# Optimization experiments

Measured on AMD Instinct MI355X. Metric: run time of the kernel, lower is better.

## Reference

```python
import jax, jax.numpy as jnp
import numpy as np

NHEADS = 4   # attention heads (search_cfg.nheads)
WS = 7       # spatial search window side -> WS*WS candidates per query
PS = 3       # patch size for distance computation (search_cfg.ps)
K = 16       # top-k neighbors kept (search_cfg.k)


def layer_norm_2d(vid, w, b, eps=1e-6):
    # LayerNorm over channel dim at every (t,h,w) location; vid (B,T,C,H,W)
    mu = vid.mean(axis=2, keepdims=True)
    var = vid.var(axis=2, keepdims=True)
    y = (vid - mu) / jnp.sqrt(var + eps)
    return y * w[None, None, :, None, None] + b[None, None, :, None, None]


def conv1x1(vid, w, b):
    # 1x1 ConvQKV projection: vid (B,T,C,H,W), w (O,C)
    return jnp.einsum('btchw,oc->btohw', vid, w) + b[None, None, :, None, None]


def box_sum(x, ps):
    # sum over centered ps x ps patch (zero pad); x (..., H, W)
    r = ps // 2
    H, W = x.shape[-2], x.shape[-1]
    xp = jnp.pad(x, [(0, 0)] * (x.ndim - 2) + [(r, r), (r, r)])
    out = jnp.zeros_like(x)
    ah, aw = x.ndim - 2, x.ndim - 1
    for dy in range(ps):
        for dx in range(ps):
            s = jax.lax.dynamic_slice_in_dim(xp, dy, H, ah)
            s = jax.lax.dynamic_slice_in_dim(s, dx, W, aw)
            out = out + s
    return out


def nl_search(q, k):
    # patch-based non-local search: q,k (B,T,HD,c,H,W)
    B, T, HD, c, H, W = q.shape
    r = WS // 2
    kp = jnp.pad(k, ((0, 0),) * 4 + ((r, r), (r, r)))  # zero pad = invalid candidates score ~0
    offs = jnp.stack(jnp.meshgrid(jnp.arange(WS), jnp.arange(WS), indexing='ij'), -1).reshape(-1, 2)

    @jax.checkpoint
    def step(carry, off):
        dy, dx = off[0], off[1]
        ksh = jax.lax.dynamic_slice(kp, (0, 0, 0, 0, dy, dx), (B, T, HD, c, H, W))
        s = (q * ksh).sum(axis=3)      # pixel inner products (B,T,HD,H,W)
        s = box_sum(s, PS)             # patch inner products
        return carry, s

    _, scores = jax.lax.scan(step, 0, offs)        # (WS*WS,B,T,HD,H,W)
    scores = jnp.moveaxis(scores, 0, -1)           # (B,T,HD,H,W,WS*WS)
    dists, inds = jax.lax.top_k(scores, K)         # top-k neighbors per query
    return dists, inds


def nl_stack(v, weights, inds):
    # gather the K selected neighbor values, weighted; v (B,T,HD,c,H,W)
    B, T, HD, c, H, W = v.shape
    r = WS // 2
    vp = jnp.pad(v, ((0, 0),) * 4 + ((r, r), (r, r)))
    Hp, Wp = H + 2 * r, W + 2 * r
    row = jnp.arange(H)[:, None, None] + inds // WS   # (B,T,HD,H,W,K)
    col = jnp.arange(W)[None, :, None] + inds % WS
    lin = (row * Wp + col).reshape(B, T, HD, 1, H * W * K)
    vf = vp.reshape(B, T, HD, c, Hp * Wp)
    g = jnp.take_along_axis(vf, jnp.broadcast_to(lin, (B, T, HD, c, H * W * K)), axis=-1)
    g = g.reshape(B, T, HD, c, H, W, K)
    g = g * weights[:, :, :, None]                    # weight each neighbor
    # -> (B*T, HD*c, K, H, W) stack for Conv3d projection
    return jnp.transpose(g, (0, 1, 2, 3, 6, 4, 5)).reshape(B * T, HD * c, K, H, W)


def proj3d(stack, w, b):
    # Conv3d(io_dim, io_dim, (K,3,3), stride=(K,1,1), pad=(0,1,1), groups=NHEADS)
    out = jax.lax.conv_general_dilated(
        stack, w, window_strides=(K, 1, 1),
        padding=((0, 0), (1, 1), (1, 1)),
        dimension_numbers=('NCDHW', 'OIDHW', 'NCDHW'),
        feature_group_count=NHEADS)
    return out[:, :, 0] + b[None, :, None, None]


def setup_inputs() -> dict:
    key = jax.random.key(0)
    ks = jax.random.split(key, 8)
    B, T, C, H, W = 1, 4, 128, 96, 96
    sc = 1.0 / np.sqrt(C)
    inp = {
        'vid': jax.random.normal(ks[0], (B, T, C, H, W), jnp.float32),
        'ln_w': jnp.ones((C,), jnp.float32),
        'ln_b': jnp.zeros((C,), jnp.float32),
        'wq': jax.random.normal(ks[1], (C, C), jnp.float32) * sc,
        'bq': jnp.zeros((C,), jnp.float32),
        'wk': jax.random.normal(ks[2], (C, C), jnp.float32) * sc,
        'bk': jnp.zeros((C,), jnp.float32),
        'wv': jax.random.normal(ks[3], (C, C), jnp.float32) * sc,
        'bv': jnp.zeros((C,), jnp.float32),
        'proj_w': jax.random.normal(ks[4], (C, C // NHEADS, K, 3, 3), jnp.float32) * 0.02,
        'proj_b': jnp.zeros((C,), jnp.float32),
    }
    return inp


def reference(vid, ln_w, ln_b, wq, bq, wk, bk, wv, bv, proj_w, proj_b):
    B, T, C, H, W = vid.shape
    x = layer_norm_2d(vid, ln_w, ln_b)
    q = conv1x1(x, wq, bq)
    k = conv1x1(x, wk, bk)
    v = conv1x1(x, wv, bv)
    hd = lambda t: t.reshape(B, T, NHEADS, C // NHEADS, H, W)
    q, k, v = hd(q), hd(k), hd(v)
    dists, inds = nl_search(q, k)                 # k-NN search
    weights = jax.nn.softmax(dists, axis=-1)      # normalize over K
    stack = nl_stack(v, weights, inds)            # neighbor stacking
    out = proj3d(stack, proj_w, proj_b)           # conv projection collapses K
    return out.reshape(B, T, C, H, W)
```

## Files before the change

### kernel.cpp

```cpp
#include <hip/hip_runtime.h>


typedef float  f32x4  __attribute__((ext_vector_type(4)));
typedef __bf16 bf16x8 __attribute__((ext_vector_type(8)));

__device__ __forceinline__ float dpp_shr1(float x) {
  return __int_as_float(__builtin_amdgcn_update_dpp(0, __float_as_int(x), 0x111, 0xf, 0xf, false));
}
__device__ __forceinline__ float dpp_shl1(float x) {
  return __int_as_float(__builtin_amdgcn_update_dpp(0, __float_as_int(x), 0x101, 0xf, 0xf, false));
}

__global__ __launch_bounds__(256) void prep_kernel(
    const float* __restrict__ wq, const float* __restrict__ wk, const float* __restrict__ wv,
    const float* __restrict__ pw, float* __restrict__ Wt, __bf16* __restrict__ pwt,
    __bf16* __restrict__ wvh) {
  int idx = blockIdx.x * 256 + threadIdx.x;
  const int NPW = 4 * 16 * 9 * 32 * 32;
  if (idx < NPW) {
    int i  = idx & 31;
    int ol = (idx >> 5) & 31;
    int d  = (idx >> 10) % 9;
    int r  = (idx >> 10) / 9;
    int kd = r & 15;
    int g  = r >> 4;
    int o  = g * 32 + ol;
    pwt[idx] = (__bf16)pw[((o * 32 + i) * 16 + kd) * 9 + d];
  } else if (idx < NPW + 128 * 384) {
    int widx = idx - NPW;
    int o = widx % 384;
    int c = widx / 384;
    const float* __restrict__ src = (o < 128) ? wq : (o < 256 ? wk : wv);
    Wt[widx] = src[(o & 127) * 128 + c];
  } else {
    int vidx = idx - NPW - 128 * 384;
    if (vidx < 128 * 128) wvh[vidx] = (__bf16)wv[vidx];
  }
}

__global__ __launch_bounds__(64) void ln_stats_kernel(
    const float* __restrict__ vid, float* __restrict__ mu, float* __restrict__ rs) {
  int pix = blockIdx.x * 64 + threadIdx.x;
  int f = blockIdx.y;
  const float* __restrict__ vp = vid + (size_t)f * 128 * 9216 + pix;
  float s = 0.f, s2 = 0.f;
  #pragma unroll 8
  for (int c = 0; c < 128; ++c) { float x = vp[(size_t)c * 9216]; s += x; s2 += x * x; }
  float m_ = s * (1.f / 128.f);
  float v_ = fmaxf(s2 * (1.f / 128.f) - m_ * m_, 0.f);
  mu[f * 9216 + pix] = m_;
  rs[f * 9216 + pix] = rsqrtf(v_ + 1e-6f);
}

__global__ __launch_bounds__(256) void xbf_kernel(
    const float* __restrict__ vid, const float* __restrict__ mu, const float* __restrict__ rs,
    const float* __restrict__ lnw, const float* __restrict__ lnb, __bf16* __restrict__ xbf) {
  __shared__ __align__(16) __bf16 tile[128 * 128];
  __shared__ float muL[128], rsL[128], lwS[128], lbS[128];
  int t = threadIdx.x;
  int pf = blockIdx.x * 128;
  int f = blockIdx.y;
  if (t < 128) { muL[t] = mu[f * 9216 + pf + t]; rsL[t] = rs[f * 9216 + pf + t]; }
  else { lwS[t - 128] = lnw[t - 128]; lbS[t - 128] = lnb[t - 128]; }
  __syncthreads();
  #pragma unroll 4
  for (int it = 0; it < 16; ++it) {
    int idx = it * 256 + t;
    int c = idx >> 5, p4 = idx & 31;
    float4 v = *(const float4*)&vid[((size_t)(f * 128 + c)) * 9216 + pf + p4 * 4];
    float xs[4] = {v.x, v.y, v.z, v.w};
    #pragma unroll
    for (int i = 0; i < 4; ++i) {
      int pix = p4 * 4 + i;
      float xn = (xs[i] - muL[pix]) * rsL[pix] * lwS[c] + lbS[c];
      int cp = c ^ (((pix >> 2) & 7) << 3);
      tile[pix * 128 + cp] = (__bf16)xn;
    }
  }
  __syncthreads();
  int pix = t >> 1, half = t & 1;
  __bf16* __restrict__ dst = xbf + ((size_t)(f * 9216) + pf + pix) * 128 + half * 64;
  #pragma unroll
  for (int cc = 0; cc < 8; ++cc) {
    int chunk = half * 8 + cc;
    int cs = chunk ^ ((pix >> 2) & 7);
    *(int4*)&dst[cc * 8] = *(const int4*)&tile[pix * 128 + cs * 8];
  }
}

__global__ __launch_bounds__(256) void qk_gemm_kernel(
    const float* __restrict__ vid, const float* __restrict__ mu, const float* __restrict__ rs,
    const float* __restrict__ lnw, const float* __restrict__ lnb,
    const float* __restrict__ Wt, const float* __restrict__ bq, const float* __restrict__ bk,
    float* __restrict__ qb, float* __restrict__ kb) {
  __shared__ __align__(16) float Xs[32][128];
  __shared__ __align__(16) float Ws[32][128];
  __shared__ float muL[128], rsL[128], lwS[128], lbS[128];
  int tid = threadIdx.x;
  int mt = blockIdx.y;
  int N0 = blockIdx.x * 128;
  int f  = mt / 72;
  int pf = (mt % 72) * 128;

  if (tid < 128) {
    muL[tid] = mu[f * 9216 + pf + tid];
    rsL[tid] = rs[f * 9216 + pf + tid];
  } else {
    int t2 = tid - 128;
    lwS[t2] = lnw[t2];
    lbS[t2] = lnb[t2];
  }

  int tx = tid & 15, ty = tid >> 4;
  int m0 = ty * 8;
  int sm = tid & 127;
  int sk0 = tid >> 7;
  float acc[8][8];
  #pragma unroll
  for (int a = 0; a < 8; ++a)
    #pragma unroll
    for (int b = 0; b < 8; ++b) acc[a][b] = 0.f;

  const size_t vbase = (size_t)f * 128 * 9216 + pf;
  float xr[16], wr[16];

  #pragma unroll
  for (int it = 0; it < 16; ++it) {
    int kk = sk0 + 2 * it;
    xr[it] = vid[vbase + (size_t)kk * 9216 + sm];
    wr[it] = Wt[(size_t)kk * 384 + N0 + sm];
  }
  __syncthreads();
  #pragma unroll
  for (int it = 0; it < 16; ++it) {
    int kk = sk0 + 2 * it;
    Xs[kk][sm] = (xr[it] - muL[sm]) * rsL[sm] * lwS[kk] + lbS[kk];
    Ws[kk][sm] = wr[it];
  }
  __syncthreads();

  for (int kc = 0; kc < 4; ++kc) {
    if (kc < 3) {
      #pragma unroll
      for (int it = 0; it < 16; ++it) {
        int kk = sk0 + 2 * it;
        int c = (kc + 1) * 32 + kk;
        xr[it] = vid[vbase + (size_t)c * 9216 + sm];
        wr[it] = Wt[(size_t)c * 384 + N0 + sm];
      }
    }
    #pragma unroll 2
    for (int kk = 0; kk < 32; ++kk) {
      float xa[8], wa[8];
      *(float4*)&xa[0] = *(const float4*)&Xs[kk][m0];
      *(float4*)&xa[4] = *(const float4*)&Xs[kk][m0 + 4];
      *(float4*)&wa[0] = *(const float4*)&Ws[kk][tx * 4];
      *(float4*)&wa[4] = *(const float4*)&Ws[kk][64 + tx * 4];
      #pragma unroll
      for (int a = 0; a < 8; ++a)
        #pragma unroll
        for (int b = 0; b < 8; ++b)
          acc[a][b] = fmaf(xa[a], wa[b], acc[a][b]);
    }
    if (kc < 3) {
      __syncthreads();
      #pragma unroll
      for (int it = 0; it < 16; ++it) {
        int kk = sk0 + 2 * it;
        int c = (kc + 1) * 32 + kk;
        Xs[kk][sm] = (xr[it] - muL[sm]) * rsL[sm] * lwS[c] + lbS[c];
        Ws[kk][sm] = wr[it];
      }
      __syncthreads();
    }
  }

  int sel = blockIdx.x;
  int nlo = tx * 4, nhi = 64 + tx * 4;
  int hlo = nlo >> 5, clo = nlo & 31;
  int hhi = nhi >> 5, chi = nhi & 31;
  const float* __restrict__ bias = (sel == 0) ? bq : bk;
  float* __restrict__ dst = (sel == 0) ? qb : kb;
  float4 blo = make_float4(bias[nlo], bias[nlo + 1], bias[nlo + 2], bias[nlo + 3]);
  float4 bhi = make_float4(bias[nhi], bias[nhi + 1], bias[nhi + 2], bias[nhi + 3]);
  size_t base_lo = (size_t)(f * 4 + hlo) * 9216 * 32 + clo;
  size_t base_hi = (size_t)(f * 4 + hhi) * 9216 * 32 + chi;
  #pragma unroll
  for (int a = 0; a < 8; ++a) {
    size_t poff = (size_t)(pf + m0 + a) * 32;
    *(float4*)&dst[base_lo + poff] = make_float4(acc[a][0] + blo.x, acc[a][1] + blo.y,
                                                 acc[a][2] + blo.z, acc[a][3] + blo.w);
    *(float4*)&dst[base_hi + poff] = make_float4(acc[a][4] + bhi.x, acc[a][5] + bhi.y,
                                                 acc[a][6] + bhi.z, acc[a][7] + bhi.w);
  }
}

__global__ __launch_bounds__(256) void vmfma_kernel(
    const __bf16* __restrict__ xbf, const __bf16* __restrict__ wvh,
    const float* __restrict__ bv, __bf16* __restrict__ vbbf) {
  __shared__ __align__(16) __bf16 XL[64 * 128];
  __shared__ __align__(16) __bf16 WL[128 * 128];
  int t = threadIdx.x;
  int bid = blockIdx.x;
  int f = bid / 144;
  int pf = (bid % 144) * 64;

  #pragma unroll
  for (int i = 0; i < 4; ++i) {
    int idx = i * 256 + t;
    int pix = idx >> 4, ck = idx & 15;
    int4 val = *(const int4*)&xbf[((size_t)(f * 9216) + pf + pix) * 128 + ck * 8];
    *(int4*)&XL[pix * 128 + ((ck ^ (pix & 7)) << 3)] = val;
  }
  #pragma unroll
  for (int i = 0; i < 8; ++i) {
    int idx = i * 256 + t;
    int o = idx >> 4, ck = idx & 15;
    int4 val = *(const int4*)&wvh[o * 128 + ck * 8];
    *(int4*)&WL[o * 128 + ((ck ^ (o & 7)) << 3)] = val;
  }
  __syncthreads();

  int lane = t & 63, w = t >> 6;
  int wm = w >> 1, wn = w & 1;
  int kg = lane >> 4, lr = lane & 15;
  f32x4 acc[2][4];
  #pragma unroll
  for (int mf = 0; mf < 2; ++mf)
    #pragma unroll
    for (int nf = 0; nf < 4; ++nf) acc[mf][nf] = (f32x4)(0.0f);

  #pragma unroll
  for (int kc = 0; kc < 4; ++kc) {
    int ck = kc * 4 + kg;
    bf16x8 a[2], b[4];
    #pragma unroll
    for (int mf = 0; mf < 2; ++mf) {
      int pix = wm * 32 + mf * 16 + lr;
      a[mf] = *(const bf16x8*)&XL[pix * 128 + ((ck ^ (pix & 7)) << 3)];
    }
    #pragma unroll
    for (int nf = 0; nf < 4; ++nf) {
      int o = wn * 64 + nf * 16 + lr;
      b[nf] = *(const bf16x8*)&WL[o * 128 + ((ck ^ (o & 7)) << 3)];
    }
    #pragma unroll
    for (int mf = 0; mf < 2; ++mf)
      #pragma unroll
      for (int nf = 0; nf < 4; ++nf)
        acc[mf][nf] = __builtin_amdgcn_mfma_f32_16x16x32_bf16(a[mf], b[nf], acc[mf][nf], 0, 0, 0);
  }

  #pragma unroll
  for (int mf = 0; mf < 2; ++mf) {
    #pragma unroll
    for (int nf = 0; nf < 4; ++nf) {
      int o = wn * 64 + nf * 16 + lr;
      int head = o >> 5, c = o & 31;
      float bias = bv[o];
      #pragma unroll
      for (int j = 0; j < 4; ++j) {
        int pix = wm * 32 + mf * 16 + kg * 4 + j;
        vbbf[((size_t)((f * 4 + head) * 9216) + pf + pix) * 32 + c] =
            (__bf16)(acc[mf][nf][j] + bias);
      }
    }
  }
}

__global__ __launch_bounds__(256, 3) void search_kernel(
    const float* __restrict__ qb, const float* __restrict__ kb,
    float* __restrict__ wgtb, int* __restrict__ indb) {
  __shared__ __align__(16) float klds[16 * 22 * 32];
  __shared__ float slds[7][256];
  int tid = threadIdx.x;
  int th = blockIdx.y;
  int tile = blockIdx.x;
  int iy0 = (tile / 7) * 14, ix0 = (tile % 7) * 14;
  const float* __restrict__ kbase = kb + (size_t)th * 9216 * 32;

  #pragma unroll
  for (int it = 0; it < 11; ++it) {
    int i = it * 256 + tid;
    int r = i / 176, rem = i % 176;
    int col = rem >> 3, c4 = rem & 7;
    int gy = iy0 - 4 + r, gx = ix0 - 4 + col;
    float4 val = make_float4(0.f, 0.f, 0.f, 0.f);
    if ((unsigned)gy < 96u && (unsigned)gx < 96u)
      val = *(const float4*)&kbase[(size_t)(gy * 96 + gx) * 32 + c4 * 4];
    int p = r * 22 + col;
    *(float4*)&klds[p * 32 + ((c4 ^ (p & 7)) << 2)] = val;
  }

  int sy = tid >> 4, sx = tid & 15;
  int qy = iy0 - 1 + sy, qx = ix0 - 1 + sx;
  bool qok = (unsigned)qy < 96u && (unsigned)qx < 96u;
  float4 qv[8];
  #pragma unroll
  for (int j = 0; j < 8; ++j) qv[j] = make_float4(0.f, 0.f, 0.f, 0.f);
  if (qok) {
    const float* __restrict__ qp = qb + ((size_t)th * 9216 + qy * 96 + qx) * 32;
    #pragma unroll
    for (int j = 0; j < 8; ++j) qv[j] = *(const float4*)&qp[j * 4];
  }
  bool inner = (sy >= 1) && (sy <= 14) && (sx >= 1) && (sx <= 14) && qok;

  float tv[16]; int tix[16];
  #pragma unroll
  for (int j = 0; j < 16; ++j) { tv[j] = -3.0e38f; tix[j] = 0; }
  __syncthreads();

  #pragma unroll 1
  for (int dy = 0; dy < 7; ++dy) {
    if (dy > 0) {
      if (tid < 176) {
        int col = tid >> 3, c4 = tid & 7;
        int r = dy + 15;
        int gy = iy0 - 4 + r, gx = ix0 - 4 + col;
        float4 val = make_float4(0.f, 0.f, 0.f, 0.f);
        if ((unsigned)gy < 96u && (unsigned)gx < 96u)
          val = *(const float4*)&kbase[(size_t)(gy * 96 + gx) * 32 + c4 * 4];
        int p = (r & 15) * 22 + col;
        *(float4*)&klds[p * 32 + ((c4 ^ (p & 7)) << 2)] = val;
      }
      __syncthreads();
    }
    float h[7];
    #pragma unroll
    for (int dx = 0; dx < 7; ++dx) {
      int p = ((sy + dy) & 15) * 22 + (sx + dx);
      const float* __restrict__ kp = &klds[p * 32];
      int sw = p & 7;
      float sdot = 0.f;
      #pragma unroll
      for (int j = 0; j < 8; ++j) {
        float4 kq = *(const float4*)&kp[(j ^ sw) << 2];
        sdot += qv[j].x * kq.x + qv[j].y * kq.y + qv[j].z * kq.z + qv[j].w * kq.w;
      }
      h[dx] = sdot + dpp_shr1(sdot) + dpp_shl1(sdot);
      slds[dx][tid] = h[dx];
    }
    __syncthreads();
    if (inner) {
      #pragma unroll
      for (int dx = 0; dx < 7; ++dx) {
        float sc = h[dx] + slds[dx][tid - 16] + slds[dx][tid + 16];
        int oi = dy * 7 + dx;
        float cv = sc; int ci = oi;
        #pragma unroll
        for (int j = 0; j < 16; ++j) {
          bool gt = cv > tv[j];
          float mx = fmaxf(tv[j], cv);
          float mn = fminf(tv[j], cv);
          int nt = gt ? ci : tix[j];
          ci = gt ? tix[j] : ci;
          tv[j] = mx; cv = mn; tix[j] = nt;
        }
      }
    }
  }

  if (inner) {
    float mx = tv[0];
    float e[16], ssum = 0.f;
    #pragma unroll
    for (int j = 0; j < 16; ++j) { e[j] = __expf(tv[j] - mx); ssum += e[j]; }
    float inv = 1.f / ssum;
    size_t base = ((size_t)th * 9216 + qy * 96 + qx) * 16;
    #pragma unroll
    for (int j = 0; j < 4; ++j) {
      *(float4*)&wgtb[base + j * 4] =
          make_float4(e[j*4] * inv, e[j*4+1] * inv, e[j*4+2] * inv, e[j*4+3] * inv);
      *(int4*)&indb[base + j * 4] = make_int4(tix[j*4], tix[j*4+1], tix[j*4+2], tix[j*4+3]);
    }
  }
}

#define STAGE_A(BUF, VR, WC) do {                                              \
  if (gact) {                                                                  \
    __bf16 tmp_[32];                                                           \
    _Pragma("unroll")                                                          \
    for (int wv_ = 0; wv_ < 4; ++wv_) {                                        \
      unsigned uu_[4] = {(unsigned)VR[wv_].x, (unsigned)VR[wv_].y,             \
                         (unsigned)VR[wv_].z, (unsigned)VR[wv_].w};            \
      _Pragma("unroll")                                                        \
      for (int j2_ = 0; j2_ < 4; ++j2_) {                                      \
        float lo_ = __uint_as_float(uu_[j2_] << 16);                           \
        float hi_ = __uint_as_float(uu_[j2_] & 0xffff0000u);                   \
        tmp_[wv_ * 8 + j2_ * 2]     = (__bf16)(lo_ * (WC));                    \
        tmp_[wv_ * 8 + j2_ * 2 + 1] = (__bf16)(hi_ * (WC));                    \
      }                                                                        \
    }                                                                          \
    __bf16* dst_ = &(BUF)[tid * 32];                                           \
    int sela_ = (tid >> 1) & 3;                                                \
    *(int4*)&dst_[(0 ^ sela_) << 3] = *(const int4*)&tmp_[0];                  \
    *(int4*)&dst_[(1 ^ sela_) << 3] = *(const int4*)&tmp_[8];                  \
    *(int4*)&dst_[(2 ^ sela_) << 3] = *(const int4*)&tmp_[16];                 \
    *(int4*)&dst_[(3 ^ sela_) << 3] = *(const int4*)&tmp_[24];                 \
  }                                                                            \
} while (0)

#define STAGE_B(BUF, KD) do {                                                  \
  const __bf16* __restrict__ bsrc_ = pwt + (size_t)(g * 16 + (KD)) * 9216;     \
  _Pragma("unroll")                                                            \
  for (int itb_ = 0; itb_ < 3; ++itb_) {                                       \
    int i_ = itb_ * 512 + tid;                                                 \
    if (i_ < 1152) {                                                           \
      int row_ = i_ >> 2, c_ = i_ & 3;                                         \
      *(int4*)&(BUF)[row_ * 32 + ((c_ ^ ((row_ >> 1) & 3)) << 3)] =            \
          *(const int4*)&bsrc_[row_ * 32 + c_ * 8];                            \
    }                                                                          \
  }                                                                            \
} while (0)

#define GATHER(VR, WC, IND, W) do {                                            \
  int ind_ = (IND);                                                            \
  VR[0] = VR[1] = VR[2] = VR[3] = make_int4(0, 0, 0, 0);                       \
  if (inb) {                                                                   \
    int ny_ = gy + ind_ / 7 - 3, nx_ = gx + ind_ % 7 - 3;                      \
    if ((unsigned)ny_ < 96u && (unsigned)nx_ < 96u) {                          \
      const int4* __restrict__ vp_ =                                           \
          (const int4*)(vbase + (size_t)(ny_ * 96 + nx_) * 32);                \
      VR[0] = vp_[0]; VR[1] = vp_[1]; VR[2] = vp_[2]; VR[3] = vp_[3];          \
    }                                                                          \
  }                                                                            \
  WC = (W);                                                                    \
} while (0)

#define MFMA_PHASE(AB, BB) do {                                                \
  _Pragma("unroll")                                                            \
  for (int dx2_ = 0; dx2_ < 3; ++dx2_) {                                       \
    bf16x8 a_[4];                                                              \
    _Pragma("unroll")                                                          \
    for (int r_ = 0; r_ < 4; ++r_) {                                           \
      int p_ = (wid * 2 + r_) * 18 + lr + dx2_;                                \
      a_[r_] = *(const bf16x8*)&(AB)[p_ * 32 + ((kg ^ ((p_ >> 1) & 3)) << 3)]; \
    }                                                                          \
    _Pragma("unroll")                                                          \
    for (int dy2_ = 0; dy2_ < 3; ++dy2_) {                                     \
      int d_ = dy2_ * 3 + dx2_;                                                \
      bf16x8 b0_ = *(const bf16x8*)&(BB)[(d_ * 32 + lr) * 32 + bswz];          \
      bf16x8 b1_ = *(const bf16x8*)&(BB)[(d_ * 32 + 16 + lr) * 32 + bswz];     \
      acc[0][0] = __builtin_amdgcn_mfma_f32_16x16x32_bf16(a_[dy2_],     b0_, acc[0][0], 0, 0, 0); \
      acc[0][1] = __builtin_amdgcn_mfma_f32_16x16x32_bf16(a_[dy2_],     b1_, acc[0][1], 0, 0, 0); \
      acc[1][0] = __builtin_amdgcn_mfma_f32_16x16x32_bf16(a_[dy2_ + 1], b0_, acc[1][0], 0, 0, 0); \
      acc[1][1] = __builtin_amdgcn_mfma_f32_16x16x32_bf16(a_[dy2_ + 1], b1_, acc[1][1], 0, 0, 0); \
    }                                                                          \
  }                                                                            \
} while (0)

__global__ __launch_bounds__(512) void proj_kernel(
    const __bf16* __restrict__ vb, const float* __restrict__ wgtb, const int* __restrict__ indb,
    const __bf16* __restrict__ pwt, const float* __restrict__ pb, float* __restrict__ outp) {
  __shared__ __align__(16) __bf16 Albuf[2][324 * 32];
  __shared__ __align__(16) __bf16 Blbuf[2][288 * 32];
  int tid = threadIdx.x;
  int bid = blockIdx.x;
  int wg = (bid & 7) * 72 + (bid >> 3);
  int th = wg / 36;
  int tile = wg % 36;
  int g = th & 3;
  int ty0 = (tile / 6) * 16, tx0 = (tile % 6) * 16;
  int lane = tid & 63, wid = tid >> 6;
  int kg = lane >> 4, lr = lane & 15;
  int bswz = (kg ^ ((lr >> 1) & 3)) << 3;

  bool gact = tid < 324;
  int ry = tid / 18, rx = tid % 18;
  int gy = ty0 - 1 + ry, gx = tx0 - 1 + rx;
  bool inb = gact && (unsigned)gy < 96u && (unsigned)gx < 96u;
  const __bf16* __restrict__ vbase = vb + (size_t)th * 9216 * 32;
  size_t pxoff = inb ? (size_t)(gy * 96 + gx) : 0;
  const int*   __restrict__ ibase = indb + ((size_t)th * 9216 + pxoff) * 16;
  const float* __restrict__ wbase = wgtb + ((size_t)th * 9216 + pxoff) * 16;

  f32x4 acc[2][2];
  acc[0][0] = (f32x4)(0.0f); acc[0][1] = (f32x4)(0.0f);
  acc[1][0] = (f32x4)(0.0f); acc[1][1] = (f32x4)(0.0f);

  int4 iw_i = make_int4(0, 0, 0, 0);
  float4 iw_w = make_float4(0.f, 0.f, 0.f, 0.f);
  int4 vr0[4], vr1[4];
  float wc0 = 0.f, wc1 = 0.f;

  if (inb) {
    iw_i = *(const int4*)&ibase[0];
    iw_w = *(const float4*)&wbase[0];
  }
  GATHER(vr0, wc0, iw_i.x, iw_w.x);
  STAGE_A(Albuf[0], vr0, wc0);
  STAGE_B(Blbuf[0], 0);
  GATHER(vr1, wc1, iw_i.y, iw_w.y);
  __syncthreads();

  #pragma unroll 1
  for (int kq = 0; kq < 4; ++kq) {
    int k4 = kq * 4;
    STAGE_A(Albuf[1], vr1, wc1);
    STAGE_B(Blbuf[1], k4 + 1);
    GATHER(vr0, wc0, iw_i.z, iw_w.z);
    MFMA_PHASE(Albuf[0], Blbuf[0]);
    __syncthreads();
    STAGE_A(Albuf[0], vr0, wc0);
    STAGE_B(Blbuf[0], k4 + 2);
    GATHER(vr1, wc1, iw_i.w, iw_w.w);
    MFMA_PHASE(Albuf[1], Blbuf[1]);
    __syncthreads();
    STAGE_A(Albuf[1], vr1, wc1);
    STAGE_B(Blbuf[1], k4 + 3);
    if (kq < 3) {
      if (inb) {
        iw_i = *(const int4*)&ibase[k4 + 4];
        iw_w = *(const float4*)&wbase[k4 + 4];
      }
      GATHER(vr0, wc0, iw_i.x, iw_w.x);
    }
    MFMA_PHASE(Albuf[0], Blbuf[0]);
    __syncthreads();
    if (kq < 3) {
      STAGE_A(Albuf[0], vr0, wc0);
      STAGE_B(Blbuf[0], k4 + 4);
      GATHER(vr1, wc1, iw_i.y, iw_w.y);
    }
    MFMA_PHASE(Albuf[1], Blbuf[1]);
    __syncthreads();
  }

  int x0 = tx0 + kg * 4;
  int f = th >> 2;
  #pragma unroll
  for (int mt = 0; mt < 2; ++mt) {
    int y = ty0 + wid * 2 + mt;
    #pragma unroll
    for (int nt = 0; nt < 2; ++nt) {
      int o = g * 32 + nt * 16 + lr;
      float bias = pb[o];
      float4 res = make_float4(acc[mt][nt][0] + bias, acc[mt][nt][1] + bias,
                               acc[mt][nt][2] + bias, acc[mt][nt][3] + bias);
      *(float4*)&outp[(size_t)(f * 128 + o) * 9216 + y * 96 + x0] = res;
    }
  }
}

extern "C" void kernel_launch(void* const* d_in, const int* in_sizes, int n_in,
                              void* d_out, int out_size, void* d_ws, size_t ws_size,
                              hipStream_t stream) {
  const float* vid = (const float*)d_in[0];
  const float* lnw = (const float*)d_in[1];
  const float* lnb = (const float*)d_in[2];
  const float* wq  = (const float*)d_in[3];
  const float* bq  = (const float*)d_in[4];
  const float* wk  = (const float*)d_in[5];
  const float* bk  = (const float*)d_in[6];
  const float* wv_ = (const float*)d_in[7];
  const float* bv  = (const float*)d_in[8];
  const float* pw  = (const float*)d_in[9];
  const float* pb  = (const float*)d_in[10];
  float* outp = (float*)d_out;

  const size_t SZ_T  = (size_t)16 * 9216 * 32 * 4;
  const size_t SZ_TB = (size_t)16 * 9216 * 32 * 2;
  const size_t SZ_W  = (size_t)16 * 9216 * 16 * 4;
  const size_t SZ_WT = 128 * 384 * 4;
  const size_t SZ_PW = (size_t)4 * 16 * 9 * 32 * 32 * 2;
  const size_t SZ_MU = (size_t)4 * 9216 * 4;
  const size_t SZ_XB = (size_t)4 * 9216 * 128 * 2;
  const size_t SZ_WV = 128 * 128 * 2;

  char* p = (char*)d_ws;
  float* qb = (float*)p;        p += SZ_T;
  float* kb = (float*)p;        p += SZ_T;
  __bf16* vbbf = (__bf16*)p;    p += SZ_TB;
  float* wgtb = (float*)p;      p += SZ_W;
  int*   indb = (int*)p;        p += SZ_W;
  float* Wt = (float*)p;        p += SZ_WT;
  __bf16* pwt = (__bf16*)p;     p += SZ_PW;
  float* mu = (float*)p;        p += SZ_MU;
  float* rs = (float*)p;        p += SZ_MU;
  __bf16* xbf = (__bf16*)p;     p += SZ_XB;
  __bf16* wvh = (__bf16*)p;

  prep_kernel<<<2560, 256, 0, stream>>>(wq, wk, wv_, pw, Wt, pwt, wvh);
  ln_stats_kernel<<<dim3(144, 4), 64, 0, stream>>>(vid, mu, rs);
  xbf_kernel<<<dim3(72, 4), 256, 0, stream>>>(vid, mu, rs, lnw, lnb, xbf);
  qk_gemm_kernel<<<dim3(2, 288), 256, 0, stream>>>(vid, mu, rs, lnw, lnb, Wt, bq, bk, qb, kb);
  vmfma_kernel<<<576, 256, 0, stream>>>(xbf, wvh, bv, vbbf);
  search_kernel<<<dim3(49, 16), 256, 0, stream>>>(qb, kb, wgtb, indb);
  proj_kernel<<<576, 512, 0, stream>>>(vbbf, wgtb, indb, pwt, pb, outp);
}
```

Measured before the change: 212.8 us.

## Merge independent kernels into two block-dispatched fat kernels

```diff
diff --git a/kernel.cpp b/kernel.cpp
--- a/kernel.cpp
+++ b/kernel.cpp
@@ -52,326 +52,333 @@
   rs[f * 9216 + pix] = rsqrtf(v_ + 1e-6f);
 }
 
-__global__ __launch_bounds__(256) void xbf_kernel(
-    const float* __restrict__ vid, const float* __restrict__ mu, const float* __restrict__ rs,
-    const float* __restrict__ lnw, const float* __restrict__ lnb, __bf16* __restrict__ xbf) {
-  __shared__ __align__(16) __bf16 tile[128 * 128];
-  __shared__ float muL[128], rsL[128], lwS[128], lbS[128];
-  int t = threadIdx.x;
-  int pf = blockIdx.x * 128;
-  int f = blockIdx.y;
-  if (t < 128) { muL[t] = mu[f * 9216 + pf + t]; rsL[t] = rs[f * 9216 + pf + t]; }
-  else { lwS[t - 128] = lnw[t - 128]; lbS[t - 128] = lnb[t - 128]; }
-  __syncthreads();
-  #pragma unroll 4
-  for (int it = 0; it < 16; ++it) {
-    int idx = it * 256 + t;
-    int c = idx >> 5, p4 = idx & 31;
-    float4 v = *(const float4*)&vid[((size_t)(f * 128 + c)) * 9216 + pf + p4 * 4];
-    float xs[4] = {v.x, v.y, v.z, v.w};
-    #pragma unroll
-    for (int i = 0; i < 4; ++i) {
-      int pix = p4 * 4 + i;
-      float xn = (xs[i] - muL[pix]) * rsL[pix] * lwS[c] + lbS[c];
-      int cp = c ^ (((pix >> 2) & 7) << 3);
-      tile[pix * 128 + cp] = (__bf16)xn;
-    }
-  }
-  __syncthreads();
-  int pix = t >> 1, half = t & 1;
-  __bf16* __restrict__ dst = xbf + ((size_t)(f * 9216) + pf + pix) * 128 + half * 64;
-  #pragma unroll
-  for (int cc = 0; cc < 8; ++cc) {
-    int chunk = half * 8 + cc;
-    int cs = chunk ^ ((pix >> 2) & 7);
-    *(int4*)&dst[cc * 8] = *(const int4*)&tile[pix * 128 + cs * 8];
-  }
-}
-
-__global__ __launch_bounds__(256) void qk_gemm_kernel(
+__global__ __launch_bounds__(256) void fat1_kernel(
     const float* __restrict__ vid, const float* __restrict__ mu, const float* __restrict__ rs,
     const float* __restrict__ lnw, const float* __restrict__ lnb,
     const float* __restrict__ Wt, const float* __restrict__ bq, const float* __restrict__ bk,
-    float* __restrict__ qb, float* __restrict__ kb) {
-  __shared__ __align__(16) float Xs[32][128];
-  __shared__ __align__(16) float Ws[32][128];
-  __shared__ float muL[128], rsL[128], lwS[128], lbS[128];
+    float* __restrict__ qb, float* __restrict__ kb, __bf16* __restrict__ xbf) {
+  __shared__ __align__(16) char smem[34816];
   int tid = threadIdx.x;
-  int mt = blockIdx.y;
-  int N0 = blockIdx.x * 128;
-  int f  = mt / 72;
-  int pf = (mt % 72) * 128;
-
-  if (tid < 128) {
-    muL[tid] = mu[f * 9216 + pf + tid];
-    rsL[tid] = rs[f * 9216 + pf + tid];
+  int bid = blockIdx.x;
+  if (bid < 576) {
+    float* Xs  = (float*)smem;
+    float* Ws  = (float*)(smem + 16384);
+    float* muL = (float*)(smem + 32768);
+    float* rsL = muL + 128;
+    float* lwS = muL + 256;
+    float* lbS = muL + 384;
+    int sel = bid & 1;
+    int mt  = bid >> 1;
+    int N0 = sel * 128;
+    int f  = mt / 72;
+    int pf = (mt % 72) * 128;
+
+    if (tid < 128) {
+      muL[tid] = mu[f * 9216 + pf + tid];
+      rsL[tid] = rs[f * 9216 + pf + tid];
+    } else {
+      int t2 = tid - 128;
+      lwS[t2] = lnw[t2];
+      lbS[t2] = lnb[t2];
+    }
+
+    int tx = tid & 15, ty = tid >> 4;
+    int m0 = ty * 8;
+    int sm = tid & 127;
+    int sk0 = tid >> 7;
+    float acc[8][8];
+    #pragma unroll
+    for (int a = 0; a < 8; ++a)
+      #pragma unroll
+      for (int b = 0; b < 8; ++b) acc[a][b] = 0.f;
+
+    const size_t vbase = (size_t)f * 128 * 9216 + pf;
+    float xr[16], wr[16];
+
+    #pragma unroll
+    for (int it = 0; it < 16; ++it) {
+      int kk = sk0 + 2 * it;
+      xr[it] = vid[vbase + (size_t)kk * 9216 + sm];
+      wr[it] = Wt[(size_t)kk * 384 + N0 + sm];
+    }
+    __syncthreads();
+    #pragma unroll
+    for (int it = 0; it < 16; ++it) {
+      int kk = sk0 + 2 * it;
+      Xs[kk * 128 + sm] = (xr[it] - muL[sm]) * rsL[sm] * lwS[kk] + lbS[kk];
+      Ws[kk * 128 + sm] = wr[it];
+    }
+    __syncthreads();
+
+    for (int kc = 0; kc < 4; ++kc) {
+      if (kc < 3) {
+        #pragma unroll
+        for (int it = 0; it < 16; ++it) {
+          int kk = sk0 + 2 * it;
+          int c = (kc + 1) * 32 + kk;
+          xr[it] = vid[vbase + (size_t)c * 9216 + sm];
+          wr[it] = Wt[(size_t)c * 384 + N0 + sm];
+        }
+      }
+      #pragma unroll 2
+      for (int kk = 0; kk < 32; ++kk) {
+        float xa[8], wa[8];
+        *(float4*)&xa[0] = *(const float4*)&Xs[kk * 128 + m0];
+        *(float4*)&xa[4] = *(const float4*)&Xs[kk * 128 + m0 + 4];
+        *(float4*)&wa[0] = *(const float4*)&Ws[kk * 128 + tx * 4];
+        *(float4*)&wa[4] = *(const float4*)&Ws[kk * 128 + 64 + tx * 4];
+        #pragma unroll
+        for (int a = 0; a < 8; ++a)
+          #pragma unroll
+          for (int b = 0; b < 8; ++b)
+            acc[a][b] = fmaf(xa[a], wa[b], acc[a][b]);
+      }
+      if (kc < 3) {
+        __syncthreads();
+        #pragma unroll
+        for (int it = 0; it < 16; ++it) {
+          int kk = sk0 + 2 * it;
+          int c = (kc + 1) * 32 + kk;
+          Xs[kk * 128 + sm] = (xr[it] - muL[sm]) * rsL[sm] * lwS[c] + lbS[c];
+          Ws[kk * 128 + sm] = wr[it];
+        }
+        __syncthreads();
+      }
+    }
+
+    int nlo = tx * 4, nhi = 64 + tx * 4;
+    int hlo = nlo >> 5, clo = nlo & 31;
+    int hhi = nhi >> 5, chi = nhi & 31;
+    const float* __restrict__ bias = (sel == 0) ? bq : bk;
+    float* __restrict__ dst = (sel == 0) ? qb : kb;
+    float4 blo = make_float4(bias[nlo], bias[nlo + 1], bias[nlo + 2], bias[nlo + 3]);
+    float4 bhi = make_float4(bias[nhi], bias[nhi + 1], bias[nhi + 2], bias[nhi + 3]);
+    size_t base_lo = (size_t)(f * 4 + hlo) * 9216 * 32 + clo;
+    size_t base_hi = (size_t)(f * 4 + hhi) * 9216 * 32 + chi;
+    #pragma unroll
+    for (int a = 0; a < 8; ++a) {
+      size_t poff = (size_t)(pf + m0 + a) * 32;
+      *(float4*)&dst[base_lo + poff] = make_float4(acc[a][0] + blo.x, acc[a][1] + blo.y,
+                                                   acc[a][2] + blo.z, acc[a][3] + blo.w);
+      *(float4*)&dst[base_hi + poff] = make_float4(acc[a][4] + bhi.x, acc[a][5] + bhi.y,
+                                                   acc[a][6] + bhi.z, acc[a][7] + bhi.w);
+    }
   } else {
-    int t2 = tid - 128;
-    lwS[t2] = lnw[t2];
-    lbS[t2] = lnb[t2];
+    __bf16* tile = (__bf16*)smem;
+    float* muL = (float*)(smem + 32768);
+    float* rsL = muL + 128;
+    float* lwS = muL + 256;
+    float* lbS = muL + 384;
+    int r = bid - 576;
+    int pf = (r % 72) * 128;
+    int f = r / 72;
+    if (tid < 128) { muL[tid] = mu[f * 9216 + pf + tid]; rsL[tid] = rs[f * 9216 + pf + tid]; }
+    else { lwS[tid - 128] = lnw[tid - 128]; lbS[tid - 128] = lnb[tid - 128]; }
+    __syncthreads();
+    #pragma unroll 4
+    for (int it = 0; it < 16; ++it) {
+      int idx = it * 256 + tid;
+      int c = idx >> 5, p4 = idx & 31;
+      float4 v = *(const float4*)&vid[((size_t)(f * 128 + c)) * 9216 + pf + p4 * 4];
+      float xs[4] = {v.x, v.y, v.z, v.w};
+      #pragma unroll
+      for (int i = 0; i < 4; ++i) {
+        int pix = p4 * 4 + i;
+        float xn = (xs[i] - muL[pix]) * rsL[pix] * lwS[c] + lbS[c];
+        int cp = c ^ (((pix >> 2) & 7) << 3);
+        tile[pix * 128 + cp] = (__bf16)xn;
+      }
+    }
+    __syncthreads();
+    int pix = tid >> 1, half = tid & 1;
+    __bf16* __restrict__ dst = xbf + ((size_t)(f * 9216) + pf + pix) * 128 + half * 64;
+    #pragma unroll
+    for (int cc = 0; cc < 8; ++cc) {
+      int chunk = half * 8 + cc;
+      int cs = chunk ^ ((pix >> 2) & 7);
+      *(int4*)&dst[cc * 8] = *(const int4*)&tile[pix * 128 + cs * 8];
+    }
   }
-
-  int tx = tid & 15, ty = tid >> 4;
-  int m0 = ty * 8;
-  int sm = tid & 127;
-  int sk0 = tid >> 7;
-  float acc[8][8];
-  #pragma unroll
-  for (int a = 0; a < 8; ++a)
-    #pragma unroll
-    for (int b = 0; b < 8; ++b) acc[a][b] = 0.f;
-
-  const size_t vbase = (size_t)f * 128 * 9216 + pf;
-  float xr[16], wr[16];
-
-  #pragma unroll
-  for (int it = 0; it < 16; ++it) {
-    int kk = sk0 + 2 * it;
-    xr[it] = vid[vbase + (size_t)kk * 9216 + sm];
-    wr[it] = Wt[(size_t)kk * 384 + N0 + sm];
-  }
-  __syncthreads();
-  #pragma unroll
-  for (int it = 0; it < 16; ++it) {
-    int kk = sk0 + 2 * it;
-    Xs[kk][sm] = (xr[it] - muL[sm]) * rsL[sm] * lwS[kk] + lbS[kk];
-    Ws[kk][sm] = wr[it];
-  }
-  __syncthreads();
-
-  for (int kc = 0; kc < 4; ++kc) {
-    if (kc < 3) {
-      #pragma unroll
-      for (int it = 0; it < 16; ++it) {
-        int kk = sk0 + 2 * it;
-        int c = (kc + 1) * 32 + kk;
-        xr[it] = vid[vbase + (size_t)c * 9216 + sm];
-        wr[it] = Wt[(size_t)c * 384 + N0 + sm];
-      }
-    }
-    #pragma unroll 2
-    for (int kk = 0; kk < 32; ++kk) {
-      float xa[8], wa[8];
-      *(float4*)&xa[0] = *(const float4*)&Xs[kk][m0];
-      *(float4*)&xa[4] = *(const float4*)&Xs[kk][m0 + 4];
-      *(float4*)&wa[0] = *(const float4*)&Ws[kk][tx * 4];
-      *(float4*)&wa[4] = *(const float4*)&Ws[kk][64 + tx * 4];
-      #pragma unroll
-      for (int a = 0; a < 8; ++a)
-        #pragma unroll
-        for (int b = 0; b < 8; ++b)
-          acc[a][b] = fmaf(xa[a], wa[b], acc[a][b]);
-    }
-    if (kc < 3) {
-      __syncthreads();
-      #pragma unroll
-      for (int it = 0; it < 16; ++it) {
-        int kk = sk0 + 2 * it;
-        int c = (kc + 1) * 32 + kk;
-        Xs[kk][sm] = (xr[it] - muL[sm]) * rsL[sm] * lwS[c] + lbS[c];
-        Ws[kk][sm] = wr[it];
-      }
-      __syncthreads();
-    }
-  }
-
-  int sel = blockIdx.x;
-  int nlo = tx * 4, nhi = 64 + tx * 4;
-  int hlo = nlo >> 5, clo = nlo & 31;
-  int hhi = nhi >> 5, chi = nhi & 31;
-  const float* __restrict__ bias = (sel == 0) ? bq : bk;
-  float* __restrict__ dst = (sel == 0) ? qb : kb;
-  float4 blo = make_float4(bias[nlo], bias[nlo + 1], bias[nlo + 2], bias[nlo + 3]);
-  float4 bhi = make_float4(bias[nhi], bias[nhi + 1], bias[nhi + 2], bias[nhi + 3]);
-  size_t base_lo = (size_t)(f * 4 + hlo) * 9216 * 32 + clo;
-  size_t base_hi = (size_t)(f * 4 + hhi) * 9216 * 32 + chi;
-  #pragma unroll
-  for (int a = 0; a < 8; ++a) {
-    size_t poff = (size_t)(pf + m0 + a) * 32;
-    *(float4*)&dst[base_lo + poff] = make_float4(acc[a][0] + blo.x, acc[a][1] + blo.y,
-                                                 acc[a][2] + blo.z, acc[a][3] + blo.w);
-    *(float4*)&dst[base_hi + poff] = make_float4(acc[a][4] + bhi.x, acc[a][5] + bhi.y,
-                                                 acc[a][6] + bhi.z, acc[a][7] + bhi.w);
-  }
-}
-
-__global__ __launch_bounds__(256) void vmfma_kernel(
+}
+
+__global__ __launch_bounds__(256, 3) void fat2_kernel(
+    const float* __restrict__ qb, const float* __restrict__ kb,
+    float* __restrict__ wgtb, int* __restrict__ indb,
     const __bf16* __restrict__ xbf, const __bf16* __restrict__ wvh,
     const float* __restrict__ bv, __bf16* __restrict__ vbbf) {
-  __shared__ __align__(16) __bf16 XL[64 * 128];
-  __shared__ __align__(16) __bf16 WL[128 * 128];
-  int t = threadIdx.x;
+  __shared__ __align__(16) char smem[52224];
+  int tid = threadIdx.x;
   int bid = blockIdx.x;
-  int f = bid / 144;
-  int pf = (bid % 144) * 64;
-
-  #pragma unroll
-  for (int i = 0; i < 4; ++i) {
-    int idx = i * 256 + t;
-    int pix = idx >> 4, ck = idx & 15;
-    int4 val = *(const int4*)&xbf[((size_t)(f * 9216) + pf + pix) * 128 + ck * 8];
-    *(int4*)&XL[pix * 128 + ((ck ^ (pix & 7)) << 3)] = val;
-  }
-  #pragma unroll
-  for (int i = 0; i < 8; ++i) {
-    int idx = i * 256 + t;
-    int o = idx >> 4, ck = idx & 15;
-    int4 val = *(const int4*)&wvh[o * 128 + ck * 8];
-    *(int4*)&WL[o * 128 + ((ck ^ (o & 7)) << 3)] = val;
-  }
-  __syncthreads();
-
-  int lane = t & 63, w = t >> 6;
-  int wm = w >> 1, wn = w & 1;
-  int kg = lane >> 4, lr = lane & 15;
-  f32x4 acc[2][4];
-  #pragma unroll
-  for (int mf = 0; mf < 2; ++mf)
-    #pragma unroll
-    for (int nf = 0; nf < 4; ++nf) acc[mf][nf] = (f32x4)(0.0f);
-
-  #pragma unroll
-  for (int kc = 0; kc < 4; ++kc) {
-    int ck = kc * 4 + kg;
-    bf16x8 a[2], b[4];
+  if (bid < 784) {
+    float* klds = (float*)smem;
+    float (*slds)[256] = (float(*)[256])(smem + 45056);
+    int tile = bid % 49;
+    int th = bid / 49;
+    int iy0 = (tile / 7) * 14, ix0 = (tile % 7) * 14;
+    const float* __restrict__ kbase = kb + (size_t)th * 9216 * 32;
+
+    #pragma unroll
+    for (int it = 0; it < 11; ++it) {
+      int i = it * 256 + tid;
+      int r = i / 176, rem = i % 176;
+      int col = rem >> 3, c4 = rem & 7;
+      int gy = iy0 - 4 + r, gx = ix0 - 4 + col;
+      float4 val = make_float4(0.f, 0.f, 0.f, 0.f);
+      if ((unsigned)gy < 96u && (unsigned)gx < 96u)
+        val = *(const float4*)&kbase[(size_t)(gy * 96 + gx) * 32 + c4 * 4];
+      int p = r * 22 + col;
+      *(float4*)&klds[p * 32 + ((c4 ^ (p & 7)) << 2)] = val;
+    }
+
+    int sy = tid >> 4, sx = tid & 15;
+    int qy = iy0 - 1 + sy, qx = ix0 - 1 + sx;
+    bool qok = (unsigned)qy < 96u && (unsigned)qx < 96u;
+    float4 qv[8];
+    #pragma unroll
+    for (int j = 0; j < 8; ++j) qv[j] = make_float4(0.f, 0.f, 0.f, 0.f);
+    if (qok) {
+      const float* __restrict__ qp = qb + ((size_t)th * 9216 + qy * 96 + qx) * 32;
+      #pragma unroll
+      for (int j = 0; j < 8; ++j) qv[j] = *(const float4*)&qp[j * 4];
+    }
+    bool inner = (sy >= 1) && (sy <= 14) && (sx >= 1) && (sx <= 14) && qok;
+
+    float tv[16]; int tix[16];
+    #pragma unroll
+    for (int j = 0; j < 16; ++j) { tv[j] = -3.0e38f; tix[j] = 0; }
+    __syncthreads();
+
+    #pragma unroll 1
+    for (int dy = 0; dy < 7; ++dy) {
+      if (dy > 0) {
+        if (tid < 176) {
+          int col = tid >> 3, c4 = tid & 7;
+          int r = dy + 15;
+          int gy = iy0 - 4 + r, gx = ix0 - 4 + col;
+          float4 val = make_float4(0.f, 0.f, 0.f, 0.f);
+          if ((unsigned)gy < 96u && (unsigned)gx < 96u)
+            val = *(const float4*)&kbase[(size_t)(gy * 96 + gx) * 32 + c4 * 4];
+          int p = (r & 15) * 22 + col;
+          *(float4*)&klds[p * 32 + ((c4 ^ (p & 7)) << 2)] = val;
+        }
+        __syncthreads();
+      }
+      float h[7];
+      #pragma unroll
+      for (int dx = 0; dx < 7; ++dx) {
+        int p = ((sy + dy) & 15) * 22 + (sx + dx);
+        const float* __restrict__ kp = &klds[p * 32];
+        int sw = p & 7;
+        float sdot = 0.f;
+        #pragma unroll
+        for (int j = 0; j < 8; ++j) {
+          float4 kq = *(const float4*)&kp[(j ^ sw) << 2];
+          sdot += qv[j].x * kq.x + qv[j].y * kq.y + qv[j].z * kq.z + qv[j].w * kq.w;
+        }
+        h[dx] = sdot + dpp_shr1(sdot) + dpp_shl1(sdot);
+        slds[dx][tid] = h[dx];
+      }
+      __syncthreads();
+      if (inner) {
+        #pragma unroll
+        for (int dx = 0; dx < 7; ++dx) {
+          float sc = h[dx] + slds[dx][tid - 16] + slds[dx][tid + 16];
+          int oi = dy * 7 + dx;
+          float cv = sc; int ci = oi;
+          #pragma unroll
+          for (int j = 0; j < 16; ++j) {
+            bool gt = cv > tv[j];
+            float mx = fmaxf(tv[j], cv);
+            float mn = fminf(tv[j], cv);
+            int nt = gt ? ci : tix[j];
+            ci = gt ? tix[j] : ci;
+            tv[j] = mx; cv = mn; tix[j] = nt;
+          }
+        }
+      }
+    }
+
+    if (inner) {
+      float mx = tv[0];
+      float e[16], ssum = 0.f;
+      #pragma unroll
+      for (int j = 0; j < 16; ++j) { e[j] = __expf(tv[j] - mx); ssum += e[j]; }
+      float inv = 1.f / ssum;
+      size_t base = ((size_t)th * 9216 + qy * 96 + qx) * 16;
+      #pragma unroll
+      for (int j = 0; j < 4; ++j) {
+        *(float4*)&wgtb[base + j * 4] =
+            make_float4(e[j*4] * inv, e[j*4+1] * inv, e[j*4+2] * inv, e[j*4+3] * inv);
+        *(int4*)&indb[base + j * 4] = make_int4(tix[j*4], tix[j*4+1], tix[j*4+2], tix[j*4+3]);
+      }
+    }
+  } else {
+    __bf16* XL = (__bf16*)smem;
+    __bf16* WL = (__bf16*)(smem + 16384);
+    int r = bid - 784;
+    int f = r / 144;
+    int pf = (r % 144) * 64;
+
+    #pragma unroll
+    for (int i = 0; i < 4; ++i) {
+      int idx = i * 256 + tid;
+      int pix = idx >> 4, ck = idx & 15;
+      int4 val = *(const int4*)&xbf[((size_t)(f * 9216) + pf + pix) * 128 + ck * 8];
+      *(int4*)&XL[pix * 128 + ((ck ^ (pix & 7)) << 3)] = val;
+    }
+    #pragma unroll
+    for (int i = 0; i < 8; ++i) {
+      int idx = i * 256 + tid;
+      int o = idx >> 4, ck = idx & 15;
+      int4 val = *(const int4*)&wvh[o * 128 + ck * 8];
+      *(int4*)&WL[o * 128 + ((ck ^ (o & 7)) << 3)] = val;
+    }
+    __syncthreads();
+
+    int lane = tid & 63, w = tid >> 6;
+    int wm = w >> 1, wn = w & 1;
+    int kg = lane >> 4, lr = lane & 15;
+    f32x4 acc[2][4];
+    #pragma unroll
+    for (int mf = 0; mf < 2; ++mf)
+      #pragma unroll
+      for (int nf = 0; nf < 4; ++nf) acc[mf][nf] = (f32x4)(0.0f);
+
+    #pragma unroll
+    for (int kc = 0; kc < 4; ++kc) {
+      int ck = kc * 4 + kg;
+      bf16x8 a[2], b[4];
+      #pragma unroll
+      for (int mf = 0; mf < 2; ++mf) {
+        int pix = wm * 32 + mf * 16 + lr;
+        a[mf] = *(const bf16x8*)&XL[pix * 128 + ((ck ^ (pix & 7)) << 3)];
+      }
+      #pragma unroll
+      for (int nf = 0; nf < 4; ++nf) {
+        int o = wn * 64 + nf * 16 + lr;
+        b[nf] = *(const bf16x8*)&WL[o * 128 + ((ck ^ (o & 7)) << 3)];
+      }
+      #pragma unroll
+      for (int mf = 0; mf < 2; ++mf)
+        #pragma unroll
+        for (int nf = 0; nf < 4; ++nf)
+          acc[mf][nf] = __builtin_amdgcn_mfma_f32_16x16x32_bf16(a[mf], b[nf], acc[mf][nf], 0, 0, 0);
+    }
+
     #pragma unroll
     for (int mf = 0; mf < 2; ++mf) {
-      int pix = wm * 32 + mf * 16 + lr;
-      a[mf] = *(const bf16x8*)&XL[pix * 128 + ((ck ^ (pix & 7)) << 3)];
-    }
-    #pragma unroll
-    for (int nf = 0; nf < 4; ++nf) {
-      int o = wn * 64 + nf * 16 + lr;
-      b[nf] = *(const bf16x8*)&WL[o * 128 + ((ck ^ (o & 7)) << 3)];
-    }
-    #pragma unroll
-    for (int mf = 0; mf < 2; ++mf)
-      #pragma unroll
-      for (int nf = 0; nf < 4; ++nf)
-        acc[mf][nf] = __builtin_amdgcn_mfma_f32_16x16x32_bf16(a[mf], b[nf], acc[mf][nf], 0, 0, 0);
-  }
-
-  #pragma unroll
-  for (int mf = 0; mf < 2; ++mf) {
-    #pragma unroll
-    for (int nf = 0; nf < 4; ++nf) {
-      int o = wn * 64 + nf * 16 + lr;
-      int head = o >> 5, c = o & 31;
-      float bias = bv[o];
-      #pragma unroll
-      for (int j = 0; j < 4; ++j) {
-        int pix = wm * 32 + mf * 16 + kg * 4 + j;
-        vbbf[((size_t)((f * 4 + head) * 9216) + pf + pix) * 32 + c] =
-            (__bf16)(acc[mf][nf][j] + bias);
-      }
-    }
-  }
-}
-
-__global__ __launch_bounds__(256, 3) void search_kernel(
-    const float* __restrict__ qb, const float* __restrict__ kb,
-    float* __restrict__ wgtb, int* __restrict__ indb) {
-  __shared__ __align__(16) float klds[16 * 22 * 32];
-  __shared__ float slds[7][256];
-  int tid = threadIdx.x;
-  int th = blockIdx.y;
-  int tile = blockIdx.x;
-  int iy0 = (tile / 7) * 14, ix0 = (tile % 7) * 14;
-  const float* __restrict__ kbase = kb + (size_t)th * 9216 * 32;
-
-  #pragma unroll
-  for (int it = 0; it < 11; ++it) {
-    int i = it * 256 + tid;
-    int r = i / 176, rem = i % 176;
-    int col = rem >> 3, c4 = rem & 7;
-    int gy = iy0 - 4 + r, gx = ix0 - 4 + col;
-    float4 val = make_float4(0.f, 0.f, 0.f, 0.f);
-    if ((unsigned)gy < 96u && (unsigned)gx < 96u)
-      val = *(const float4*)&kbase[(size_t)(gy * 96 + gx) * 32 + c4 * 4];
-    int p = r * 22 + col;
-    *(float4*)&klds[p * 32 + ((c4 ^ (p & 7)) << 2)] = val;
-  }
-
-  int sy = tid >> 4, sx = tid & 15;
-  int qy = iy0 - 1 + sy, qx = ix0 - 1 + sx;
-  bool qok = (unsigned)qy < 96u && (unsigned)qx < 96u;
-  float4 qv[8];
-  #pragma unroll
-  for (int j = 0; j < 8; ++j) qv[j] = make_float4(0.f, 0.f, 0.f, 0.f);
-  if (qok) {
-    const float* __restrict__ qp = qb + ((size_t)th * 9216 + qy * 96 + qx) * 32;
-    #pragma unroll
-    for (int j = 0; j < 8; ++j) qv[j] = *(const float4*)&qp[j * 4];
-  }
-  bool inner = (sy >= 1) && (sy <= 14) && (sx >= 1) && (sx <= 14) && qok;
-
-  float tv[16]; int tix[16];
-  #pragma unroll
-  for (int j = 0; j < 16; ++j) { tv[j] = -3.0e38f; tix[j] = 0; }
-  __syncthreads();
-
-  #pragma unroll 1
-  for (int dy = 0; dy < 7; ++dy) {
-    if (dy > 0) {
-      if (tid < 176) {
-        int col = tid >> 3, c4 = tid & 7;
-        int r = dy + 15;
-        int gy = iy0 - 4 + r, gx = ix0 - 4 + col;
-        float4 val = make_float4(0.f, 0.f, 0.f, 0.f);
-        if ((unsigned)gy < 96u && (unsigned)gx < 96u)
-          val = *(const float4*)&kbase[(size_t)(gy * 96 + gx) * 32 + c4 * 4];
-        int p = (r & 15) * 22 + col;
-        *(float4*)&klds[p * 32 + ((c4 ^ (p & 7)) << 2)] = val;
-      }
-      __syncthreads();
-    }
-    float h[7];
-    #pragma unroll
-    for (int dx = 0; dx < 7; ++dx) {
-      int p = ((sy + dy) & 15) * 22 + (sx + dx);
-      const float* __restrict__ kp = &klds[p * 32];
-      int sw = p & 7;
-      float sdot = 0.f;
-      #pragma unroll
-      for (int j = 0; j < 8; ++j) {
-        float4 kq = *(const float4*)&kp[(j ^ sw) << 2];
-        sdot += qv[j].x * kq.x + qv[j].y * kq.y + qv[j].z * kq.z + qv[j].w * kq.w;
-      }
-      h[dx] = sdot + dpp_shr1(sdot) + dpp_shl1(sdot);
-      slds[dx][tid] = h[dx];
-    }
-    __syncthreads();
-    if (inner) {
-      #pragma unroll
-      for (int dx = 0; dx < 7; ++dx) {
-        float sc = h[dx] + slds[dx][tid - 16] + slds[dx][tid + 16];
-        int oi = dy * 7 + dx;
-        float cv = sc; int ci = oi;
-        #pragma unroll
-        for (int j = 0; j < 16; ++j) {
-          bool gt = cv > tv[j];
-          float mx = fmaxf(tv[j], cv);
-          float mn = fminf(tv[j], cv);
-          int nt = gt ? ci : tix[j];
-          ci = gt ? tix[j] : ci;
-          tv[j] = mx; cv = mn; tix[j] = nt;
+      #pragma unroll
+      for (int nf = 0; nf < 4; ++nf) {
+        int o = wn * 64 + nf * 16 + lr;
+        int head = o >> 5, c = o & 31;
+        float bias = bv[o];
+        #pragma unroll
+        for (int j = 0; j < 4; ++j) {
+          int pix = wm * 32 + mf * 16 + kg * 4 + j;
+          vbbf[((size_t)((f * 4 + head) * 9216) + pf + pix) * 32 + c] =
+              (__bf16)(acc[mf][nf][j] + bias);
         }
       }
-    }
-  }
-
-  if (inner) {
-    float mx = tv[0];
-    float e[16], ssum = 0.f;
-    #pragma unroll
-    for (int j = 0; j < 16; ++j) { e[j] = __expf(tv[j] - mx); ssum += e[j]; }
-    float inv = 1.f / ssum;
-    size_t base = ((size_t)th * 9216 + qy * 96 + qx) * 16;
-    #pragma unroll
-    for (int j = 0; j < 4; ++j) {
-      *(float4*)&wgtb[base + j * 4] =
-          make_float4(e[j*4] * inv, e[j*4+1] * inv, e[j*4+2] * inv, e[j*4+3] * inv);
-      *(int4*)&indb[base + j * 4] = make_int4(tix[j*4], tix[j*4+1], tix[j*4+2], tix[j*4+3]);
     }
   }
 }
@@ -582,9 +589,7 @@
 
   prep_kernel<<<2560, 256, 0, stream>>>(wq, wk, wv_, pw, Wt, pwt, wvh);
   ln_stats_kernel<<<dim3(144, 4), 64, 0, stream>>>(vid, mu, rs);
-  xbf_kernel<<<dim3(72, 4), 256, 0, stream>>>(vid, mu, rs, lnw, lnb, xbf);
-  qk_gemm_kernel<<<dim3(2, 288), 256, 0, stream>>>(vid, mu, rs, lnw, lnb, Wt, bq, bk, qb, kb);
-  vmfma_kernel<<<576, 256, 0, stream>>>(xbf, wvh, bv, vbbf);
-  search_kernel<<<dim3(49, 16), 256, 0, stream>>>(qb, kb, wgtb, indb);
+  fat1_kernel<<<864, 256, 0, stream>>>(vid, mu, rs, lnw, lnb, Wt, bq, bk, qb, kb, xbf);
+  fat2_kernel<<<1360, 256, 0, stream>>>(qb, kb, wgtb, indb, xbf, wvh, bv, vbbf);
   proj_kernel<<<576, 512, 0, stream>>>(vbbf, wgtb, indb, pwt, pb, outp);
 }
```

New measurement: 195.0 us. 8.4% less time.
